# Performance work log

Measured on AMD Instinct MI355X. Metric: run time of the kernel, lower is better.

The kernel has to match this reference:

```python
import jax, jax.numpy as jnp
import numpy as np

V, C, M, O, E = 100000, 64, 8, 64, 1200000


def setup_inputs() -> dict:
    key = jax.random.key(0)
    ks = jax.random.split(key, 8)
    data = jax.random.normal(ks[0], (V, C), dtype=jnp.float32)
    edge_src = jax.random.randint(ks[1], (E,), 0, V)  # receiver vertex i
    edge_dst = jax.random.randint(ks[2], (E,), 0, V)  # neighbor vertex j
    edge_weight = jax.random.uniform(ks[3], (E,), dtype=jnp.float32)  # neighbors[i,j]
    std = 0.1  # TruncatedNormal(stddev=0.1) init
    var_u = jax.random.truncated_normal(ks[4], -2.0, 2.0, (C, M), jnp.float32) * std
    var_c = jax.random.truncated_normal(ks[5], -2.0, 2.0, (M,), jnp.float32) * std
    var_w = jax.random.truncated_normal(ks[6], -2.0, 2.0, (M, C, O), jnp.float32) * std
    var_b = jax.random.truncated_normal(ks[7], -2.0, 2.0, (O,), jnp.float32) * std
    return dict(data=data, edge_src=edge_src, edge_dst=edge_dst,
                edge_weight=edge_weight, var_u=var_u, var_c=var_c,
                var_w=var_w, var_b=var_b)


def reference(data, edge_src, edge_dst, edge_weight, var_u, var_c, var_w, var_b):
    # FeaStNet feature-steered convolution, translation invariant (var_v = -var_u):
    #   q_m(i,j) = softmax_m( u_m . (x_i - x_j) + c_m )
    #   y_i = b + sum_j neighbors[i,j] * sum_m q_m(i,j) * (W_m x_j)
    num_m, out_ch = var_w.shape[0], var_w.shape[2]
    xu = data @ var_u                                   # [V, M]
    logits = xu[edge_src] - xu[edge_dst] + var_c        # [E, M]
    q = jax.nn.softmax(logits, axis=-1)                 # [E, M] per-edge soft assignment
    x_j = data[edge_dst] * edge_weight[:, None]         # [E, C] weighted neighbor features
    out = jnp.zeros((data.shape[0], out_ch), dtype=data.dtype)
    for m in range(num_m):  # small fixed loop over M=8 weight matrices
        agg = jax.ops.segment_sum(x_j * q[:, m:m + 1], edge_src,
                                  num_segments=data.shape[0])  # [V, C]
        out = out + agg @ var_w[m]                      # [V, O]
    return out + var_b
```

## Files before the change

kernel.cpp:

```cpp
#include <hip/hip_runtime.h>
#include <hip/hip_bf16.h>
#include <hip/hip_fp16.h>

#define C_DIM 64
#define M_DIM 8
#define O_DIM 64
#define KSLOT 48
#define OVF_CAP 65536

typedef _Float16 h8 __attribute__((ext_vector_type(8)));
typedef float f32x4 __attribute__((ext_vector_type(4)));

union HH { __half2 h2; unsigned int u; _Float16 f2[2]; };

__device__ __forceinline__ unsigned int packh2(float a, float b) {
    HH x;
    x.f2[0] = (_Float16)a;
    x.f2[1] = (_Float16)b;
    return x.u;
}
__device__ __forceinline__ int rfl(int x) { return __builtin_amdgcn_readfirstlane(x); }

__global__ __launch_bounds__(256) void prep_kernel(
    const float* __restrict__ data, const float* __restrict__ u,
    const int* __restrict__ esrc, const int* __restrict__ edst,
    const float* __restrict__ ew, const float* __restrict__ w,
    _Float16* __restrict__ xuh, unsigned short* __restrict__ datah,
    int* __restrict__ counts, uint2* __restrict__ recs,
    int* __restrict__ ovf_cnt, int* __restrict__ ovf,
    _Float16* __restrict__ bfrag, int V, int E) {
    int b = blockIdx.x, t = threadIdx.x;
    if (b < 16) {
        int tt = b * 256 + t;
        int kt = tt >> 8;
        int rem = tt & 255;
        int nt = rem >> 6;
        int lane = rem & 63;
        int quad = lane >> 4;
        int n = nt * 16 + (lane & 15);
#pragma unroll
        for (int j = 0; j < 8; ++j) {
            int k = kt * 32 + quad * 8 + j;
            bfrag[(size_t)tt * 8 + j] = (_Float16)w[k * 64 + n];
        }
    }
    int v = b * 32 + (t >> 3), m = t & 7;
    if (v < V) {
        const float* dr = data + (size_t)v * C_DIM;
        float s = 0.f;
#pragma unroll
        for (int c = 0; c < C_DIM; ++c) s = fmaf(dr[c], u[c * M_DIM + m], s);
        xuh[(size_t)v * 8 + m] = (_Float16)s;
    }
    size_t base = (size_t)b * 2048 + (size_t)t * 8;
    if (base + 7 < (size_t)V * C_DIM) {
        f32x4 x0 = *(const f32x4*)&data[base];
        f32x4 x1 = *(const f32x4*)&data[base + 4];
        uint4 o;
        o.x = packh2(x0[0], x0[1]);
        o.y = packh2(x0[2], x0[3]);
        o.z = packh2(x1[0], x1[1]);
        o.w = packh2(x1[2], x1[3]);
        *(uint4*)&datah[base] = o;
    }
    int e = b * 256 + t;
    if (e < E) {
        int s = esrc[e];
        int rank = atomicAdd(&counts[s], 1);
        if (rank < KSLOT) {
            uint2 r;
            r.x = (unsigned int)edst[e];
            r.y = __float_as_uint(ew[e]);
            recs[(size_t)s * KSLOT + rank] = r;
        } else {
            int oi = atomicAdd(ovf_cnt, 1);
            if (oi < OVF_CAP) ovf[oi] = e;
        }
    }
}

#define A_STRIDE 520
__global__ __launch_bounds__(256) void fused_kernel(
    const unsigned short* __restrict__ datah, const uint2* __restrict__ recs,
    const _Float16* __restrict__ xuh, const float* __restrict__ vc,
    const int* __restrict__ counts, const _Float16* __restrict__ bfragG,
    const float* __restrict__ bias, float* __restrict__ out, int V) {
    __shared__ _Float16 At[16 * A_STRIDE];
    __shared__ int ebj[4][64];
    __shared__ uint4 ebq[4][64];
    __shared__ float xscS[4][4][8];
    __shared__ int pS[4][5];
    __shared__ int oS[4][4];
    int wave = rfl(threadIdx.x >> 6);
    int lane = threadIdx.x & 63;
    int v_base = blockIdx.x * 16;
    int v0 = v_base + wave * 4;

    if (lane < 4) {
        int v = v0 + lane;
        int dd = (v < V) ? min(counts[v], KSLOT) : 0;
        oS[wave][lane] = v * KSLOT;
        pS[wave][lane + 1] = dd;
    }
    if (lane == 0) {
        pS[wave][0] = 0;
        int s = 0;
#pragma unroll
        for (int i = 1; i <= 4; ++i) {
            s += pS[wave][i];
            pS[wave][i] = s;
        }
    }
    if (lane < 32) {
        int i = lane >> 3, m = lane & 7;
        int v = v0 + i;
        float s = 0.f;
        if (v < V) s = (float)xuh[(size_t)v0 * 8 + lane] + vc[m];
        xscS[wave][i][m] = s;
    }

    HH z; z.u = 0;
    __half2 acc[4][4];
#pragma unroll
    for (int i = 0; i < 4; ++i)
#pragma unroll
        for (int k = 0; k < 4; ++k) acc[i][k] = z.h2;

    int total = rfl(pS[wave][4]);

    for (int c0 = 0; c0 < total; c0 += 64) {
        int g = c0 + lane;
        if (g < total) {
            int p1 = pS[wave][1], p2 = pS[wave][2], p3 = pS[wave][3];
            int r = (g >= p1) + (g >= p2) + (g >= p3);
            int pr = (r > 0) ? ((r > 1) ? ((r > 2) ? p3 : p2) : p1) : 0;
            int ob = oS[wave][r];
            int pos = ob + (g - pr);
            uint2 rec = recs[pos];
            int j = (int)rec.x;
            float w = __uint_as_float(rec.y);
            f32x4 xa = *(const f32x4*)&xscS[wave][r][0];
            f32x4 xb = *(const f32x4*)&xscS[wave][r][4];
            uint4 xr = *(const uint4*)&xuh[(size_t)j * 8];
            HH a2, b2, c2, d2;
            a2.u = xr.x; b2.u = xr.y; c2.u = xr.z; d2.u = xr.w;
            float lg[8];
            lg[0] = xa[0] - (float)a2.f2[0];
            lg[1] = xa[1] - (float)a2.f2[1];
            lg[2] = xa[2] - (float)b2.f2[0];
            lg[3] = xa[3] - (float)b2.f2[1];
            lg[4] = xb[0] - (float)c2.f2[0];
            lg[5] = xb[1] - (float)c2.f2[1];
            lg[6] = xb[2] - (float)d2.f2[0];
            lg[7] = xb[3] - (float)d2.f2[1];
            float mx = -1e30f;
#pragma unroll
            for (int m = 0; m < 8; ++m) mx = fmaxf(mx, lg[m]);
            float den = 0.f;
#pragma unroll
            for (int m = 0; m < 8; ++m) {
                lg[m] = __expf(lg[m] - mx);
                den += lg[m];
            }
            float inv = w / den;
#pragma unroll
            for (int m = 0; m < 8; ++m) lg[m] *= inv;
            uint4 qp;
            qp.x = packh2(lg[0], lg[1]);
            qp.y = packh2(lg[2], lg[3]);
            qp.z = packh2(lg[4], lg[5]);
            qp.w = packh2(lg[6], lg[7]);
            ebj[wave][lane] = j;
            ebq[wave][lane] = qp;
        }
#define CONSUME2(rr, qv, xsv)                                                  \
    do {                                                                       \
        HH q01, q23, q45, q67, xx;                                             \
        q01.u = (qv).x; q23.u = (qv).y;                                        \
        q45.u = (qv).z; q67.u = (qv).w;                                        \
        unsigned int xv_ = (unsigned int)(xsv);                                \
        xx.u = xv_ | (xv_ << 16);                                              \
        acc[rr][0] = __hfma2(xx.h2, q01.h2, acc[rr][0]);                       \
        acc[rr][1] = __hfma2(xx.h2, q23.h2, acc[rr][1]);                       \
        acc[rr][2] = __hfma2(xx.h2, q45.h2, acc[rr][2]);                       \
        acc[rr][3] = __hfma2(xx.h2, q67.h2, acc[rr][3]);                       \
    } while (0)
#pragma unroll
        for (int r2 = 0; r2 < 4; ++r2) {
            int pr0 = rfl(pS[wave][r2]);
            int pr1 = rfl(pS[wave][r2 + 1]);
            int lo2 = max(pr0, c0);
            int hi2 = min(pr1, c0 + 64);
            int n = hi2 - lo2;
            if (n <= 0) continue;
            int tb = lo2 - c0;
            int tt = 0;
            for (; tt + 8 <= n; tt += 8) {
                int jj[8];
                uint4 qq[8];
                unsigned short xs[8];
#pragma unroll
                for (int u = 0; u < 8; ++u) {
                    jj[u] = rfl(ebj[wave][tb + tt + u]);
                    qq[u] = ebq[wave][tb + tt + u];
                }
#pragma unroll
                for (int u = 0; u < 8; ++u) {
                    const unsigned short* xp = datah + ((size_t)jj[u] << 6);
                    xs[u] = xp[lane];
                }
#pragma unroll
                for (int u = 0; u < 8; ++u) CONSUME2(r2, qq[u], xs[u]);
            }
            for (; tt + 4 <= n; tt += 4) {
                int jj[4];
                uint4 qq[4];
                unsigned short xs[4];
#pragma unroll
                for (int u = 0; u < 4; ++u) {
                    jj[u] = rfl(ebj[wave][tb + tt + u]);
                    qq[u] = ebq[wave][tb + tt + u];
                }
#pragma unroll
                for (int u = 0; u < 4; ++u) {
                    const unsigned short* xp = datah + ((size_t)jj[u] << 6);
                    xs[u] = xp[lane];
                }
#pragma unroll
                for (int u = 0; u < 4; ++u) CONSUME2(r2, qq[u], xs[u]);
            }
            for (; tt < n; ++tt) {
                int j0 = rfl(ebj[wave][tb + tt]);
                uint4 qv = ebq[wave][tb + tt];
                const unsigned short* xp = datah + ((size_t)j0 << 6);
                unsigned short xs0 = xp[lane];
                CONSUME2(r2, qv, xs0);
            }
        }
    }

#pragma unroll
    for (int i = 0; i < 4; ++i) {
        int row = wave * 4 + i;
        HH a01, a23, a45, a67;
        a01.h2 = acc[i][0]; a23.h2 = acc[i][1];
        a45.h2 = acc[i][2]; a67.h2 = acc[i][3];
        _Float16* Ar = &At[row * A_STRIDE + lane];
        Ar[0 * 64] = a01.f2[0];
        Ar[1 * 64] = a01.f2[1];
        Ar[2 * 64] = a23.f2[0];
        Ar[3 * 64] = a23.f2[1];
        Ar[4 * 64] = a45.f2[0];
        Ar[5 * 64] = a45.f2[1];
        Ar[6 * 64] = a67.f2[0];
        Ar[7 * 64] = a67.f2[1];
    }
    __syncthreads();

    f32x4 cacc = {0.f, 0.f, 0.f, 0.f};
    int quad = lane >> 4;
    int r16 = lane & 15;
#pragma unroll
    for (int kt = 0; kt < 16; ++kt) {
        h8 a = *(const h8*)&At[r16 * A_STRIDE + kt * 32 + quad * 8];
        h8 b = *(const h8*)&bfragG[((size_t)(kt * 4 + wave) * 64 + lane) * 8];
        cacc = __builtin_amdgcn_mfma_f32_16x16x32_f16(a, b, cacc, 0, 0, 0);
    }
#pragma unroll
    for (int r = 0; r < 4; ++r) {
        int row = quad * 4 + r;
        int v = v_base + row;
        if (v < V) {
            int o = wave * 16 + r16;
            out[(size_t)v * 64 + o] = cacc[r] + bias[o];
        }
    }
}

__global__ __launch_bounds__(256) void cleanup_kernel(
    const int* __restrict__ ovf_cnt, const int* __restrict__ ovf,
    const int* __restrict__ esrc, const int* __restrict__ edst,
    const float* __restrict__ ew, const _Float16* __restrict__ xuh,
    const float* __restrict__ vc, const float* __restrict__ var_w,
    const unsigned short* __restrict__ datah, float* __restrict__ out) {
    int n = min(*ovf_cnt, OVF_CAP);
    int nw = gridDim.x * (blockDim.x >> 6);
    int wid = blockIdx.x * (blockDim.x >> 6) + (threadIdx.x >> 6);
    int lane = threadIdx.x & 63;
    for (int i = wid; i < n; i += nw) {
        int e = ovf[i];
        int s = esrc[e], j = edst[e];
        float w = ew[e];
        float lg[8];
        float mx = -1e30f;
#pragma unroll
        for (int m = 0; m < 8; ++m) {
            lg[m] = (float)xuh[(size_t)s * 8 + m] - (float)xuh[(size_t)j * 8 + m] + vc[m];
            mx = fmaxf(mx, lg[m]);
        }
        float den = 0.f;
#pragma unroll
        for (int m = 0; m < 8; ++m) {
            lg[m] = __expf(lg[m] - mx);
            den += lg[m];
        }
        float inv = w / den;
        float t = 0.f;
#pragma unroll
        for (int m = 0; m < 8; ++m) {
            float sum = 0.f;
            for (int c = 0; c < C_DIM; ++c) {
                HH x;
                x.u = (unsigned int)datah[(size_t)j * 64 + c];
                sum = fmaf((float)x.f2[0], var_w[((size_t)m * 64 + c) * 64 + lane], sum);
            }
            t = fmaf(lg[m] * inv, sum, t);
        }
        atomicAdd(&out[(size_t)s * 64 + lane], t);
    }
}

extern "C" void kernel_launch(void* const* d_in, const int* in_sizes, int n_in,
                              void* d_out, int out_size, void* d_ws, size_t ws_size,
                              hipStream_t stream) {
    const float* data  = (const float*)d_in[0];
    const int*   esrc  = (const int*)d_in[1];
    const int*   edst  = (const int*)d_in[2];
    const float* ew    = (const float*)d_in[3];
    const float* var_u = (const float*)d_in[4];
    const float* var_c = (const float*)d_in[5];
    const float* var_w = (const float*)d_in[6];
    const float* var_b = (const float*)d_in[7];
    float* out = (float*)d_out;

    int V = in_sizes[0] / C_DIM;
    int E = in_sizes[1];

    char* ws = (char*)d_ws;
    size_t off = 0;
    auto alloc = [&](size_t bytes) -> void* {
        void* p = ws + off;
        off = (off + bytes + 255) & ~(size_t)255;
        return p;
    };
    size_t zbytes = (size_t)V * 4 + 256;
    char* zr = (char*)alloc(zbytes);
    int* counts  = (int*)zr;
    int* ovf_cnt = (int*)(zr + (size_t)V * 4);

    _Float16*  xuh   = (_Float16*)alloc((size_t)V * 8 * 2);
    int*       ovf   = (int*)alloc((size_t)OVF_CAP * 4);
    uint2*     recs  = (uint2*)alloc((size_t)V * KSLOT * 8);
    _Float16*  bfrag = (_Float16*)alloc((size_t)512 * 64 * 2);
    unsigned short* datah = (unsigned short*)alloc((size_t)V * 64 * 2);

    hipMemsetAsync(zr, 0, zbytes, stream);

    int pb = (E + 255) / 256;
    prep_kernel<<<pb, 256, 0, stream>>>(data, var_u, esrc, edst, ew, var_w,
                                        xuh, datah, counts, recs, ovf_cnt, ovf,
                                        bfrag, V, E);
    fused_kernel<<<(V + 15) / 16, 256, 0, stream>>>(datah, recs, xuh, var_c,
                                                    counts, bfrag, var_b, out, V);
    cleanup_kernel<<<8, 256, 0, stream>>>(ovf_cnt, ovf, esrc, edst, ew, xuh,
                                          var_c, var_w, datah, out);
}
```

Baseline: 217.2 us.

## Replace global-atomic edge binning with two-level bucketed staging and placement

Edge bucketing by source vertex moves from one global atomicAdd per edge to a two-pass scheme. First, 256 blocks stage edges in LDS per 512-vertex bucket and flush them in chunks to a per-block pool. Then a place kernel, one block per bucket, ranks edges with LDS atomics and writes the per-vertex slots. KSLOT shrinks to 28 and overflow records become self-contained (src, dst, weight), so cleanup no longer re-reads the edge arrays. This trades scattered global atomics for an extra kernel launch and pool traffic, and it relies on the uniform degree distribution to keep overflow small.

```diff
diff --git a/kernel.cpp b/kernel.cpp
--- a/kernel.cpp
+++ b/kernel.cpp
@@ -5,8 +5,14 @@
 #define C_DIM 64
 #define M_DIM 8
 #define O_DIM 64
-#define KSLOT 48
-#define OVF_CAP 65536
+#define KSLOT 28
+#define OVF_CAP 32768
+
+#define G1 256
+#define BSHIFT 9
+#define NBMAX 208
+#define SCAP 16
+#define CAP_PB 36
 
 typedef _Float16 h8 __attribute__((ext_vector_type(8)));
 typedef float f32x4 __attribute__((ext_vector_type(4)));
@@ -26,12 +32,90 @@
     const int* __restrict__ esrc, const int* __restrict__ edst,
     const float* __restrict__ ew, const float* __restrict__ w,
     _Float16* __restrict__ xuh, unsigned short* __restrict__ datah,
-    int* __restrict__ counts, uint2* __restrict__ recs,
-    int* __restrict__ ovf_cnt, int* __restrict__ ovf,
-    _Float16* __restrict__ bfrag, int V, int E) {
+    uint2* __restrict__ pool, int* __restrict__ gpb,
+    int* __restrict__ ovf_cnt, uint4* __restrict__ ovf,
+    _Float16* __restrict__ bfrag, int V, int E, int nb) {
+    __shared__ uint2 stg[NBMAX][SCAP];
+    __shared__ int scnt[NBMAX];
+    __shared__ int fcnt[NBMAX];
     int b = blockIdx.x, t = threadIdx.x;
-    if (b < 16) {
-        int tt = b * 256 + t;
+
+    if (b < G1) {
+        for (int i = t; i < NBMAX; i += 256) { scnt[i] = 0; fcnt[i] = 0; }
+        __syncthreads();
+        int per = (E + G1 - 1) / G1;
+        int eBeg = b * per;
+        int eEnd = min(E, eBeg + per);
+        int iters = (per + 255) >> 8;
+        for (int it = 0; it < iters; ++it) {
+            int e = eBeg + it * 256 + t;
+            if (e < eEnd) {
+                int s = esrc[e];
+                int bk = s >> BSHIFT;
+                uint2 rec;
+                rec.x = (unsigned int)edst[e] | ((unsigned int)(s & 511) << 17);
+                rec.y = __float_as_uint(ew[e]);
+                int r = atomicAdd(&scnt[bk], 1);
+                if (r < SCAP) {
+                    stg[bk][r] = rec;
+                } else {
+                    int fr = atomicAdd(&fcnt[bk], 1);
+                    if (fr < CAP_PB) {
+                        pool[((size_t)bk * G1 + b) * CAP_PB + fr] = rec;
+                    } else {
+                        int oi = atomicAdd(ovf_cnt, 1);
+                        if (oi < OVF_CAP) {
+                            uint4 o4;
+                            o4.x = (unsigned int)s;
+                            o4.y = rec.x & 0x1FFFFu;
+                            o4.z = rec.y;
+                            o4.w = 0;
+                            ovf[oi] = o4;
+                        }
+                    }
+                }
+            }
+            __syncthreads();
+            bool last = (it == iters - 1);
+            if (t < nb) {
+                int n = min(scnt[t], SCAP);
+                int nf = last ? n : (n & ~7);
+                if (nf > 0) {
+                    int base = fcnt[t];
+                    int room = CAP_PB - base;
+                    if (room < 0) room = 0;
+                    int take = min(nf, room);
+                    uint2* dst = &pool[((size_t)t * G1 + b) * CAP_PB + base];
+                    for (int k = 0; k < take; ++k) dst[k] = stg[t][k];
+                    for (int k = take; k < nf; ++k) {
+                        int oi = atomicAdd(ovf_cnt, 1);
+                        if (oi < OVF_CAP) {
+                            uint2 rr = stg[t][k];
+                            uint4 o4;
+                            o4.x = (unsigned int)((t << BSHIFT) + (int)(rr.x >> 17));
+                            o4.y = rr.x & 0x1FFFFu;
+                            o4.z = rr.y;
+                            o4.w = 0;
+                            ovf[oi] = o4;
+                        }
+                    }
+                    fcnt[t] = base + take;
+                    int rem = n - nf;
+                    for (int k = 0; k < rem; ++k) stg[t][k] = stg[t][nf + k];
+                    scnt[t] = rem;
+                }
+            }
+            __syncthreads();
+        }
+        if (t < nb) {
+            int fc = fcnt[t];
+            gpb[t * G1 + b] = (fc < CAP_PB) ? fc : CAP_PB;
+        }
+        return;
+    }
+
+    if (b < G1 + 16) {
+        int tt = (b - G1) * 256 + t;
         int kt = tt >> 8;
         int rem = tt & 255;
         int nt = rem >> 6;
@@ -43,8 +127,11 @@
             int k = kt * 32 + quad * 8 + j;
             bfrag[(size_t)tt * 8 + j] = (_Float16)w[k * 64 + n];
         }
-    }
-    int v = b * 32 + (t >> 3), m = t & 7;
+        return;
+    }
+
+    int vb = b - (G1 + 16);
+    int v = vb * 32 + (t >> 3), m = t & 7;
     if (v < V) {
         const float* dr = data + (size_t)v * C_DIM;
         float s = 0.f;
@@ -52,7 +139,7 @@
         for (int c = 0; c < C_DIM; ++c) s = fmaf(dr[c], u[c * M_DIM + m], s);
         xuh[(size_t)v * 8 + m] = (_Float16)s;
     }
-    size_t base = (size_t)b * 2048 + (size_t)t * 8;
+    size_t base = (size_t)vb * 2048 + (size_t)t * 8;
     if (base + 7 < (size_t)V * C_DIM) {
         f32x4 x0 = *(const f32x4*)&data[base];
         f32x4 x1 = *(const f32x4*)&data[base + 4];
@@ -63,20 +150,52 @@
         o.w = packh2(x1[2], x1[3]);
         *(uint4*)&datah[base] = o;
     }
-    int e = b * 256 + t;
-    if (e < E) {
-        int s = esrc[e];
-        int rank = atomicAdd(&counts[s], 1);
-        if (rank < KSLOT) {
-            uint2 r;
-            r.x = (unsigned int)edst[e];
-            r.y = __float_as_uint(ew[e]);
-            recs[(size_t)s * KSLOT + rank] = r;
-        } else {
-            int oi = atomicAdd(ovf_cnt, 1);
-            if (oi < OVF_CAP) ovf[oi] = e;
-        }
-    }
+}
+
+__global__ __launch_bounds__(256) void place_kernel(
+    const uint2* __restrict__ pool, const int* __restrict__ gpb,
+    uint2* __restrict__ recs, int* __restrict__ counts,
+    int* __restrict__ ovf_cnt, uint4* __restrict__ ovf, int V) {
+    __shared__ int vcnt[512];
+    __shared__ int cnts[G1];
+    int b = blockIdx.x, t = threadIdx.x;
+    vcnt[t] = 0;
+    vcnt[t + 256] = 0;
+    cnts[t] = gpb[b * G1 + t];
+    __syncthreads();
+    int wave = t >> 6, lane = t & 63;
+    for (int sec = wave; sec < G1; sec += 4) {
+        int ns = cnts[sec];
+        if (ns > CAP_PB) ns = CAP_PB;
+        if (lane < ns) {
+            uint2 rec = pool[((size_t)b * G1 + sec) * CAP_PB + lane];
+            int low = (int)(rec.x >> 17);
+            int dst = (int)(rec.x & 0x1FFFFu);
+            int r = atomicAdd(&vcnt[low], 1);
+            int v = (b << BSHIFT) + low;
+            if (r < KSLOT) {
+                uint2 o;
+                o.x = (unsigned int)dst;
+                o.y = rec.y;
+                recs[(size_t)v * KSLOT + r] = o;
+            } else {
+                int oi = atomicAdd(ovf_cnt, 1);
+                if (oi < OVF_CAP) {
+                    uint4 o4;
+                    o4.x = (unsigned int)v;
+                    o4.y = (unsigned int)dst;
+                    o4.z = rec.y;
+                    o4.w = 0;
+                    ovf[oi] = o4;
+                }
+            }
+        }
+    }
+    __syncthreads();
+    int v0 = (b << BSHIFT) + t;
+    if (v0 < V) counts[v0] = vcnt[t] < KSLOT ? vcnt[t] : KSLOT;
+    int v1 = v0 + 256;
+    if (v1 < V) counts[v1] = vcnt[t + 256] < KSLOT ? vcnt[t + 256] : KSLOT;
 }
 
 #define A_STRIDE 520
@@ -278,19 +397,18 @@
 }
 
 __global__ __launch_bounds__(256) void cleanup_kernel(
-    const int* __restrict__ ovf_cnt, const int* __restrict__ ovf,
-    const int* __restrict__ esrc, const int* __restrict__ edst,
-    const float* __restrict__ ew, const _Float16* __restrict__ xuh,
-    const float* __restrict__ vc, const float* __restrict__ var_w,
-    const unsigned short* __restrict__ datah, float* __restrict__ out) {
+    const int* __restrict__ ovf_cnt, const uint4* __restrict__ ovf,
+    const _Float16* __restrict__ xuh, const float* __restrict__ vc,
+    const float* __restrict__ var_w, const unsigned short* __restrict__ datah,
+    float* __restrict__ out) {
     int n = min(*ovf_cnt, OVF_CAP);
     int nw = gridDim.x * (blockDim.x >> 6);
     int wid = blockIdx.x * (blockDim.x >> 6) + (threadIdx.x >> 6);
     int lane = threadIdx.x & 63;
     for (int i = wid; i < n; i += nw) {
-        int e = ovf[i];
-        int s = esrc[e], j = edst[e];
-        float w = ew[e];
+        uint4 r4 = ovf[i];
+        int s = (int)r4.x, j = (int)r4.y;
+        float w = __uint_as_float(r4.z);
         float lg[8];
         float mx = -1e30f;
 #pragma unroll
@@ -335,6 +453,7 @@
 
     int V = in_sizes[0] / C_DIM;
     int E = in_sizes[1];
+    int nb = (V + 511) >> BSHIFT;
 
     char* ws = (char*)d_ws;
     size_t off = 0;
@@ -343,25 +462,29 @@
         off = (off + bytes + 255) & ~(size_t)255;
         return p;
     };
-    size_t zbytes = (size_t)V * 4 + 256;
-    char* zr = (char*)alloc(zbytes);
-    int* counts  = (int*)zr;
-    int* ovf_cnt = (int*)(zr + (size_t)V * 4);
+    int* ovf_cnt = (int*)alloc(256);
 
     _Float16*  xuh   = (_Float16*)alloc((size_t)V * 8 * 2);
-    int*       ovf   = (int*)alloc((size_t)OVF_CAP * 4);
+    uint4*     ovf   = (uint4*)alloc((size_t)OVF_CAP * 16);
     uint2*     recs  = (uint2*)alloc((size_t)V * KSLOT * 8);
     _Float16*  bfrag = (_Float16*)alloc((size_t)512 * 64 * 2);
     unsigned short* datah = (unsigned short*)alloc((size_t)V * 64 * 2);
-
-    hipMemsetAsync(zr, 0, zbytes, stream);
-
-    int pb = (E + 255) / 256;
-    prep_kernel<<<pb, 256, 0, stream>>>(data, var_u, esrc, edst, ew, var_w,
-                                        xuh, datah, counts, recs, ovf_cnt, ovf,
-                                        bfrag, V, E);
+    uint2*     pool  = (uint2*)alloc((size_t)nb * G1 * CAP_PB * 8);
+    int*       gpb   = (int*)alloc((size_t)nb * G1 * 4);
+    int*       counts = (int*)alloc((size_t)V * 4);
+
+    hipMemsetAsync(ovf_cnt, 0, 256, stream);
+
+    int sb = (V * C_DIM + 2047) >> 11;
+    int xb = (V + 31) >> 5;
+    int streamb = sb > xb ? sb : xb;
+    int g1 = G1 + 16 + streamb;
+    prep_kernel<<<g1, 256, 0, stream>>>(data, var_u, esrc, edst, ew, var_w,
+                                        xuh, datah, pool, gpb, ovf_cnt, ovf,
+                                        bfrag, V, E, nb);
+    place_kernel<<<nb, 256, 0, stream>>>(pool, gpb, recs, counts, ovf_cnt, ovf, V);
     fused_kernel<<<(V + 15) / 16, 256, 0, stream>>>(datah, recs, xuh, var_c,
                                                     counts, bfrag, var_b, out, V);
-    cleanup_kernel<<<8, 256, 0, stream>>>(ovf_cnt, ovf, esrc, edst, ew, xuh,
-                                          var_c, var_w, datah, out);
-}
+    cleanup_kernel<<<64, 256, 0, stream>>>(ovf_cnt, ovf, xuh, var_c, var_w,
+                                           datah, out);
+}
```

After: 281.8 us. 29.8% more time.
